# Kernel optimization log

Measured on AMD Instinct MI355X. Metric: run time of the kernel, lower is better.

## Reference

```python
import jax, jax.numpy as jnp
import numpy as np
from jax import lax

SPATIAL = 4
PAD = 1
STRIDE = 1


def _route(x, rconv_w, rconv_b, fc_w, fc_b, num_experts):
    # x: (b, c, h, w); adaptive avg pool to (SPATIAL, SPATIAL) -- h,w divisible by SPATIAL
    b, c, h, w = x.shape
    pooled = x.reshape(b, c, SPATIAL, h // SPATIAL, SPATIAL, w // SPATIAL).mean(axis=(3, 5))
    # 1x1 conv: (b,c,s,s) x (rc,c) -> (b,rc,s,s)
    y = jnp.einsum('bcij,rc->brij', pooled, rconv_w) + rconv_b[None, :, None, None]
    y = jax.nn.relu(y).reshape(b, -1)                      # (b, rc*s*s)
    y = jax.nn.relu(y @ fc_w.T + fc_b)                     # (b, num_experts*c)
    y = y.reshape(b, num_experts, c)
    return jax.nn.sigmoid(y)                               # (b, k, c)


def _conv_per_sample(xi, wi):
    # xi: (c_in, h, w), wi: (c_out, c_in, kh, kw)
    out = lax.conv_general_dilated(
        xi[None], wi, window_strides=(STRIDE, STRIDE),
        padding=[(PAD, PAD), (PAD, PAD)],
        dimension_numbers=('NCHW', 'OIHW', 'NCHW'))
    return out[0]


def setup_inputs() -> dict:
    key = jax.random.key(0)
    ks = jax.random.split(key, 6)
    b, c_in, c_out, kk, ne = 16, 256, 256, 3, 3
    rc = max(c_in // 16, 16)  # reduction_channels = 16
    x = jax.random.normal(ks[0], (b, c_in, 64, 64), dtype=jnp.float32)
    expert_weight = jax.random.normal(ks[1], (ne, c_out, c_in, kk, kk), dtype=jnp.float32) * 0.02
    rconv_w = jax.random.normal(ks[2], (rc, c_in), dtype=jnp.float32) * 0.05
    rconv_b = jax.random.normal(ks[3], (rc,), dtype=jnp.float32) * 0.05
    fc_w = jax.random.normal(ks[4], (ne * c_in, rc * SPATIAL * SPATIAL), dtype=jnp.float32) * 0.05
    fc_b = jax.random.normal(ks[5], (ne * c_in,), dtype=jnp.float32) * 0.05
    return {"x": x, "expert_weight": expert_weight, "rconv_w": rconv_w,
            "rconv_b": rconv_b, "fc_w": fc_w, "fc_b": fc_b}


def reference(x, expert_weight, rconv_w, rconv_b, fc_w, fc_b):
    ne = expert_weight.shape[0]
    r = _route(x, rconv_w, rconv_b, fc_w, fc_b, ne)        # (b, k, c_in)
    # per-sample combined weights: routing scales input channels of each expert kernel
    w = jnp.einsum('bkc,kocij->bocij', r, expert_weight)    # (b, c_out, c_in, kh, kw)
    out = jax.vmap(_conv_per_sample)(x, w)                  # (b, c_out, h', w')
    return out
```

## Files before the change

kernel.cpp:

```cpp
#include <hip/hip_runtime.h>

#define B_   16
#define C_   256
#define OC_  256
#define H_   64
#define W_   64

typedef __attribute__((ext_vector_type(8))) __bf16 bf16x8;
typedef __attribute__((ext_vector_type(4))) float  f32x4;

__device__ __forceinline__ short f2bf(float f) {
    unsigned u = __float_as_uint(f);
    u += 0x7fffu + ((u >> 16) & 1u);
    return (short)(u >> 16);
}
__device__ __forceinline__ unsigned pk2(float a, float b) {
    return (unsigned(f2bf(a)) & 0xffffu) | (unsigned(f2bf(b)) << 16);
}
__device__ __forceinline__ void gll16(const void* g, void* l) {
    __builtin_amdgcn_global_load_lds(
        (const __attribute__((address_space(1))) unsigned int*)g,
        (__attribute__((address_space(3))) unsigned int*)l,
        16, 0, 0);
}

__global__ __launch_bounds__(256) void k_transpose_pool(
        const float* __restrict__ x, short* __restrict__ xt, float* __restrict__ pooled) {
    int y = blockIdx.x, b = blockIdx.y, t = threadIdx.x;
    int si = y >> 4;
    int lane = t & 63, wv = t >> 6;
    int xq = lane & 15, cw = lane >> 4;
    __shared__ float tile[64 * 67];

    for (int cc = 0; cc < 4; ++cc) {
        int cbase = cc * 64;
        if (cc) __syncthreads();
        #pragma unroll
        for (int r = 0; r < 4; ++r) {
            int c_l = r * 16 + wv * 4 + cw;
            float4 v = *(const float4*)&x[(((size_t)b * C_ + cbase + c_l) * H_ + y) * W_ + xq * 4];
            float* tp = &tile[c_l * 67 + xq * 4];
            tp[0] = v.x; tp[1] = v.y; tp[2] = v.z; tp[3] = v.w;
            float s = v.x + v.y + v.z + v.w;
            s += __shfl_xor(s, 1);
            s += __shfl_xor(s, 2);
            if ((lane & 3) == 0)
                atomicAdd(&pooled[((b * 4 + si) * 4 + (xq >> 2)) * 256 + cbase + c_l], s);
        }
        __syncthreads();
        #pragma unroll
        for (int r2 = 0; r2 < 2; ++r2) {
            int u = r2 * 256 + t;
            int xx = u >> 3, cgl = u & 7;
            float f[8];
            #pragma unroll
            for (int j = 0; j < 8; ++j) f[j] = tile[(cgl * 8 + j) * 67 + xx];
            uint4 pkv;
            pkv.x = pk2(f[0], f[1]); pkv.y = pk2(f[2], f[3]);
            pkv.z = pk2(f[4], f[5]); pkv.w = pk2(f[6], f[7]);
            *(uint4*)&xt[(((size_t)b * H_ + y) * W_ + xx) * C_ + cbase + cgl * 8] = pkv;
        }
    }
}

__global__ __launch_bounds__(256) void k_route(
        const float* __restrict__ pooled, const float* __restrict__ rconv_w,
        const float* __restrict__ rconv_b, const float* __restrict__ fc_w,
        const float* __restrict__ fc_b, float* __restrict__ r_buf) {
    int b = blockIdx.x >> 2;
    int slice = blockIdx.x & 3;
    int t = threadIdx.x;
    int lane = t & 63, wv = t >> 6;
    __shared__ float pl[16][257];
    __shared__ float y1[256];

    #pragma unroll
    for (int q = 0; q < 16; ++q)
        pl[q][t] = pooled[b * 4096 + q * 256 + t] * (1.0f / 256.0f);
    __syncthreads();
    {
        int rcc = t >> 4, ss = t & 15;
        float acc = rconv_b[rcc];
        #pragma unroll 8
        for (int c = 0; c < 256; ++c)
            acc += pl[ss][c] * rconv_w[rcc * 256 + c];
        y1[rcc * 16 + ss] = fmaxf(acc, 0.f);
    }
    __syncthreads();
    #pragma unroll 4
    for (int i = 0; i < 48; ++i) {
        int e = slice * 192 + wv * 48 + i;
        const float* row = fc_w + (size_t)e * 256;
        float p = y1[lane]       * row[lane]
                + y1[lane + 64]  * row[lane + 64]
                + y1[lane + 128] * row[lane + 128]
                + y1[lane + 192] * row[lane + 192];
        #pragma unroll
        for (int d = 1; d < 64; d <<= 1)
            p += __shfl_xor(p, d);
        if (lane == 0) {
            float a = fmaxf(p + fc_b[e], 0.f);
            r_buf[(size_t)b * 768 + e] = 1.f / (1.f + __expf(-a));
        }
    }
}

__global__ __launch_bounds__(256) void k_combine(
        const float* __restrict__ E, const float* __restrict__ r_buf,
        short* __restrict__ wcomb) {
    int o = blockIdx.x;
    int b0 = blockIdx.y * 4;
    int t = threadIdx.x;
    __shared__ float eT[3][2304];
    #pragma unroll
    for (int k = 0; k < 3; ++k)
        #pragma unroll
        for (int q = 0; q < 9; ++q)
            eT[k][q * 256 + t] = E[((size_t)k * OC_ + o) * 2304 + q * 256 + t];
    __syncthreads();
    int c = t;
    #pragma unroll
    for (int bb = 0; bb < 4; ++bb) {
        int b = b0 + bb;
        float r0 = r_buf[(size_t)b * 768 + c];
        float r1 = r_buf[(size_t)b * 768 + 256 + c];
        float r2 = r_buf[(size_t)b * 768 + 512 + c];
        short* wo = wcomb + ((size_t)(b * OC_ + o) * 9) * C_;
        #pragma unroll
        for (int tap = 0; tap < 9; ++tap) {
            float v = r0 * eT[0][c * 9 + tap] + r1 * eT[1][c * 9 + tap]
                    + r2 * eT[2][c * 9 + tap];
            wo[tap * C_ + c] = f2bf(v);
        }
    }
}

__global__ __launch_bounds__(256, 2) void k_conv(
        const short* __restrict__ xt, const short* __restrict__ wcomb,
        float* __restrict__ out, const short* __restrict__ zbuf) {
    int lin  = blockIdx.x;
    int work = (lin & 7) * 64 + (lin >> 3);
    int b      = work >> 5;
    int o_base = ((work >> 4) & 1) * 128;
    int y0     = (work & 15) * 4;

    int t = threadIdx.x;
    int lane = t & 63, w = t >> 6;
    int quad = lane >> 4, l15 = lane & 15;

    __shared__ __align__(16) short win[6 * 64 * 64];
    __shared__ __align__(16) short abuf[2][128 * 64];

    int zoff = (int)(zbuf - xt);

    int woff[12];
    #pragma unroll
    for (int r = 0; r < 12; ++r) {
        int u = r * 256 + t;
        int pos = u >> 3, sp = u & 7;
        int wrow = pos >> 6, xc = pos & 63;
        int yy = y0 - 1 + wrow;
        int ss = sp ^ (xc & 7);
        woff[r] = ((unsigned)yy < 64u)
            ? ((b * 64 + yy) * 64 + xc) * 256 + ss * 8
            : zoff;
    }
    int aoff[4];
    #pragma unroll
    for (int r = 0; r < 4; ++r) {
        int u = r * 256 + t;
        int o_l = u >> 3, sp = u & 7;
        int ss = sp ^ (o_l & 7);
        aoff[r] = ((b * 256 + o_base + o_l) * 9) * 256 + ss * 8;
    }

    int m_base = (w & 1) * 64;
    int ry0    = (w >> 1) * 2;

    f32x4 acc[4][8];
    #pragma unroll
    for (int i = 0; i < 4; ++i)
        #pragma unroll
        for (int j = 0; j < 8; ++j) acc[i][j] = {0.f, 0.f, 0.f, 0.f};

    for (int cc = 0; cc < 4; ++cc) {
        int ccOff = cc * 64;
        #pragma unroll
        for (int r = 0; r < 12; ++r)
            gll16(xt + woff[r] + ccOff, &win[(r * 256 + w * 64) * 8]);
        #pragma unroll
        for (int r = 0; r < 4; ++r)
            gll16(wcomb + aoff[r] + ccOff, &abuf[0][(r * 256 + w * 64) * 8]);
        __syncthreads();

        #pragma unroll
        for (int tap = 0; tap < 9; ++tap) {
            const int ti = tap / 3, tj = tap % 3;
            const int cur = tap & 1;
            if (tap < 8) {
                int off2 = (tap + 1) * 256 + ccOff;
                #pragma unroll
                for (int r = 0; r < 4; ++r)
                    gll16(wcomb + aoff[r] + off2, &abuf[cur ^ 1][(r * 256 + w * 64) * 8]);
            }
            #pragma unroll
            for (int s = 0; s < 2; ++s) {
                int slog = s * 4 + quad;
                bf16x8 af[4], bv[8];
                #pragma unroll
                for (int mb = 0; mb < 4; ++mb) {
                    int o_l = m_base + mb * 16 + l15;
                    af[mb] = *(const bf16x8*)&abuf[cur][o_l * 64 + ((slog ^ (o_l & 7)) * 8)];
                }
                #pragma unroll
                for (int nb = 0; nb < 8; ++nb) {
                    int rr = nb >> 2, xq4 = nb & 3;
                    int xc = xq4 * 16 + l15 + (tj - 1);
                    bool ok = ((unsigned)xc < 64u);
                    int xs = ok ? xc : 0;
                    int wrow = ry0 + rr + ti;
                    bf16x8 v = *(const bf16x8*)&win[(wrow * 64 + xs) * 64
                                                    + ((slog ^ (xs & 7)) * 8)];
                    bf16x8 zz = {};
                    bv[nb] = ok ? v : zz;
                }
                __builtin_amdgcn_s_setprio(1);
                #pragma unroll
                for (int mb = 0; mb < 4; ++mb)
                    #pragma unroll
                    for (int nb = 0; nb < 8; ++nb)
                        acc[mb][nb] = __builtin_amdgcn_mfma_f32_16x16x32_bf16(
                            af[mb], bv[nb], acc[mb][nb], 0, 0, 0);
                __builtin_amdgcn_s_setprio(0);
            }
            __syncthreads();
        }
    }

    #pragma unroll
    for (int mb = 0; mb < 4; ++mb) {
        #pragma unroll
        for (int nb = 0; nb < 8; ++nb) {
            int rr = nb >> 2, xq4 = nb & 3;
            int xx = xq4 * 16 + l15;
            int yy = y0 + ry0 + rr;
            #pragma unroll
            for (int rg = 0; rg < 4; ++rg) {
                int o = o_base + m_base + mb * 16 + quad * 4 + rg;
                out[(((size_t)b * OC_ + o) * H_ + yy) * W_ + xx] = acc[mb][nb][rg];
            }
        }
    }
}

extern "C" void kernel_launch(void* const* d_in, const int* in_sizes, int n_in,
                              void* d_out, int out_size, void* d_ws, size_t ws_size,
                              hipStream_t stream) {
    const float* x       = (const float*)d_in[0];
    const float* E       = (const float*)d_in[1];
    const float* rconv_w = (const float*)d_in[2];
    const float* rconv_b = (const float*)d_in[3];
    const float* fc_w    = (const float*)d_in[4];
    const float* fc_b    = (const float*)d_in[5];
    float* out = (float*)d_out;

    char* ws = (char*)d_ws;
    short* xt     = (short*)(ws);
    short* wcomb  = (short*)(ws + 33554432);
    float* pooled = (float*)(ws + 52428800);
    short* zbuf   = (short*)(ws + 52690944);
    float* rbuf   = (float*)(ws + 52692992);

    hipMemsetAsync(pooled, 0, 262144 + 1024, stream);

    k_transpose_pool<<<dim3(64, 16), 256, 0, stream>>>(x, xt, pooled);
    k_route<<<dim3(64), 256, 0, stream>>>(pooled, rconv_w, rconv_b, fc_w, fc_b, rbuf);
    k_combine<<<dim3(256, 4), 256, 0, stream>>>(E, rbuf, wcomb);
    k_conv<<<dim3(512), 256, 0, stream>>>(xt, wcomb, out, zbuf);
}
```

Baseline: 251.4 us.

## Pre-swizzle combined weights into MFMA fragment order and load directly to registers

The combine kernel now writes the per-sample bf16 weights in a layout where each wave's 16x32 A-fragment for a given tap, channel chunk and sub-step is a contiguous 1 KB block. The conv kernel drops the LDS double buffer for weights and instead prefetches A-fragments straight from global into registers two phases ahead. This also removes the per-tap __syncthreads, leaving only one barrier per channel chunk. It relies on L2/global latency being hidden by the register prefetch distance, and it raises register pressure.

```diff
diff --git a/kernel.cpp b/kernel.cpp
--- a/kernel.cpp
+++ b/kernel.cpp
@@ -119,18 +119,21 @@
             eT[k][q * 256 + t] = E[((size_t)k * OC_ + o) * 2304 + q * 256 + t];
     __syncthreads();
     int c = t;
+    int ccs = (c >> 5);
+    int sub = ((c >> 3) & 3) * 128 + (o & 15) * 8 + (c & 7);
+    int og  = o >> 4;
     #pragma unroll
     for (int bb = 0; bb < 4; ++bb) {
         int b = b0 + bb;
         float r0 = r_buf[(size_t)b * 768 + c];
         float r1 = r_buf[(size_t)b * 768 + 256 + c];
         float r2 = r_buf[(size_t)b * 768 + 512 + c];
-        short* wo = wcomb + ((size_t)(b * OC_ + o) * 9) * C_;
+        short* wo = wcomb + (size_t)b * 589824;
         #pragma unroll
         for (int tap = 0; tap < 9; ++tap) {
             float v = r0 * eT[0][c * 9 + tap] + r1 * eT[1][c * 9 + tap]
                     + r2 * eT[2][c * 9 + tap];
-            wo[tap * C_ + c] = f2bf(v);
+            wo[((tap * 8 + ccs) * 16 + og) * 512 + sub] = f2bf(v);
         }
     }
 }
@@ -149,7 +152,6 @@
     int quad = lane >> 4, l15 = lane & 15;
 
     __shared__ __align__(16) short win[6 * 64 * 64];
-    __shared__ __align__(16) short abuf[2][128 * 64];
 
     int zoff = (int)(zbuf - xt);
 
@@ -165,18 +167,13 @@
             ? ((b * 64 + yy) * 64 + xc) * 256 + ss * 8
             : zoff;
     }
-    int aoff[4];
-    #pragma unroll
-    for (int r = 0; r < 4; ++r) {
-        int u = r * 256 + t;
-        int o_l = u >> 3, sp = u & 7;
-        int ss = sp ^ (o_l & 7);
-        aoff[r] = ((b * 256 + o_base + o_l) * 9) * 256 + ss * 8;
-    }
 
     int m_base = (w & 1) * 64;
     int ry0    = (w >> 1) * 2;
 
+    const short* pA = wcomb + (size_t)b * 589824
+                    + ((o_base + m_base) >> 4) * 512 + lane * 8;
+
     f32x4 acc[4][8];
     #pragma unroll
     for (int i = 0; i < 4; ++i)
@@ -185,56 +182,57 @@
 
     for (int cc = 0; cc < 4; ++cc) {
         int ccOff = cc * 64;
+        int ccA   = cc * 16384;
         #pragma unroll
         for (int r = 0; r < 12; ++r)
             gll16(xt + woff[r] + ccOff, &win[(r * 256 + w * 64) * 8]);
-        #pragma unroll
-        for (int r = 0; r < 4; ++r)
-            gll16(wcomb + aoff[r] + ccOff, &abuf[0][(r * 256 + w * 64) * 8]);
+
+        bf16x8 P[2][4];
+        #pragma unroll
+        for (int mb = 0; mb < 4; ++mb) {
+            P[0][mb] = *(const bf16x8*)(pA + ccA + mb * 512);
+            P[1][mb] = *(const bf16x8*)(pA + ccA + 8192 + mb * 512);
+        }
         __syncthreads();
 
         #pragma unroll
-        for (int tap = 0; tap < 9; ++tap) {
-            const int ti = tap / 3, tj = tap % 3;
-            const int cur = tap & 1;
-            if (tap < 8) {
-                int off2 = (tap + 1) * 256 + ccOff;
+        for (int ph = 0; ph < 18; ++ph) {
+            const int tp = ph >> 1, s = ph & 1;
+            const int ti = tp / 3, tj = tp % 3;
+            const int cur = ph & 1;
+            int slog = s * 4 + quad;
+
+            bf16x8 bv[8];
+            #pragma unroll
+            for (int nb = 0; nb < 8; ++nb) {
+                int rr = nb >> 2, xq4 = nb & 3;
+                int xc = xq4 * 16 + l15 + (tj - 1);
+                bool ok = ((unsigned)xc < 64u);
+                int xs = ok ? xc : 0;
+                int wrow = ry0 + rr + ti;
+                bf16x8 v = *(const bf16x8*)&win[(wrow * 64 + xs) * 64
+                                                + ((slog ^ (xs & 7)) * 8)];
+                bf16x8 zz = {};
+                bv[nb] = ok ? v : zz;
+            }
+            __builtin_amdgcn_s_setprio(1);
+            #pragma unroll
+            for (int mb = 0; mb < 4; ++mb)
                 #pragma unroll
-                for (int r = 0; r < 4; ++r)
-                    gll16(wcomb + aoff[r] + off2, &abuf[cur ^ 1][(r * 256 + w * 64) * 8]);
-            }
-            #pragma unroll
-            for (int s = 0; s < 2; ++s) {
-                int slog = s * 4 + quad;
-                bf16x8 af[4], bv[8];
-                #pragma unroll
-                for (int mb = 0; mb < 4; ++mb) {
-                    int o_l = m_base + mb * 16 + l15;
-                    af[mb] = *(const bf16x8*)&abuf[cur][o_l * 64 + ((slog ^ (o_l & 7)) * 8)];
-                }
-                #pragma unroll
-                for (int nb = 0; nb < 8; ++nb) {
-                    int rr = nb >> 2, xq4 = nb & 3;
-                    int xc = xq4 * 16 + l15 + (tj - 1);
-                    bool ok = ((unsigned)xc < 64u);
-                    int xs = ok ? xc : 0;
-                    int wrow = ry0 + rr + ti;
-                    bf16x8 v = *(const bf16x8*)&win[(wrow * 64 + xs) * 64
-                                                    + ((slog ^ (xs & 7)) * 8)];
-                    bf16x8 zz = {};
-                    bv[nb] = ok ? v : zz;
-                }
-                __builtin_amdgcn_s_setprio(1);
+                for (int nb = 0; nb < 8; ++nb)
+                    acc[mb][nb] = __builtin_amdgcn_mfma_f32_16x16x32_bf16(
+                        P[cur][mb], bv[nb], acc[mb][nb], 0, 0, 0);
+            __builtin_amdgcn_s_setprio(0);
+
+            if (ph < 16) {
+                const int np = ph + 2, ntp = np >> 1, ns = np & 1;
                 #pragma unroll
                 for (int mb = 0; mb < 4; ++mb)
-                    #pragma unroll
-                    for (int nb = 0; nb < 8; ++nb)
-                        acc[mb][nb] = __builtin_amdgcn_mfma_f32_16x16x32_bf16(
-                            af[mb], bv[nb], acc[mb][nb], 0, 0, 0);
-                __builtin_amdgcn_s_setprio(0);
+                    P[cur][mb] = *(const bf16x8*)(pA + ccA + ntp * 65536
+                                                  + ns * 8192 + mb * 512);
             }
-            __syncthreads();
-        }
+        }
+        if (cc < 3) __syncthreads();
     }
 
     #pragma unroll
```

Result: slower. 256.7 us (+2.1%).
